# Kernel tuning notes

Hardware: AMD Instinct MI355X
Metric: run time of the kernel (lower is better)

Reference implementation:

```python
import jax, jax.numpy as jnp
import numpy as np

B, DIM, HEADS, AGENT = 32, 768, 12, 49
H0 = W0 = 28
N = H0 * W0


def setup_inputs() -> dict:
    key = jax.random.key(0)
    ks = jax.random.split(key, 24)
    p = lambda i, shape: jax.random.normal(ks[i], shape, jnp.float32) * 0.02
    return {
        "rgb_fea": jax.random.normal(ks[0], (B, N, DIM), jnp.float32),
        "depth_fea": jax.random.normal(ks[1], (B, N, DIM), jnp.float32),
        "rgb_q_w": p(2, (DIM, DIM)), "rgb_kv_w": p(3, (DIM, 2 * DIM)),
        "rgb_proj_w": p(4, (DIM, DIM)), "rgb_proj_b": jnp.zeros((DIM,), jnp.float32),
        "depth_q_w": p(5, (DIM, DIM)), "depth_kv_w": p(6, (DIM, 2 * DIM)),
        "depth_proj_w": p(7, (DIM, DIM)), "depth_proj_b": jnp.zeros((DIM,), jnp.float32),
        "rgb_dwc_w": p(8, (3, 3, 1, DIM)), "rgb_dwc_b": jnp.zeros((DIM,), jnp.float32),
        "depth_dwc_w": p(9, (3, 3, 1, DIM)), "depth_dwc_b": jnp.zeros((DIM,), jnp.float32),
        "rgb_an_bias": p(10, (HEADS, AGENT, 7, 7)), "rgb_na_bias": p(11, (HEADS, AGENT, 7, 7)),
        "rgb_ah_bias": p(12, (1, HEADS, AGENT, H0, 1)), "rgb_aw_bias": p(13, (1, HEADS, AGENT, 1, W0)),
        "rgb_ha_bias": p(14, (1, HEADS, H0, 1, AGENT)), "rgb_wa_bias": p(15, (1, HEADS, 1, W0, AGENT)),
        "depth_an_bias": p(16, (HEADS, AGENT, 7, 7)), "depth_na_bias": p(17, (HEADS, AGENT, 7, 7)),
        "depth_ah_bias": p(18, (1, HEADS, AGENT, H0, 1)), "depth_aw_bias": p(19, (1, HEADS, AGENT, 1, W0)),
        "depth_ha_bias": p(20, (1, HEADS, H0, 1, AGENT)), "depth_wa_bias": p(21, (1, HEADS, 1, W0, AGENT)),
        "H": H0, "W": W0,
    }


def _dwc(x, w, bias):
    # depthwise 3x3 conv, padding=1. x: [b,H,W,c], w: [3,3,1,c]
    y = jax.lax.conv_general_dilated(
        x, w, (1, 1), "SAME",
        dimension_numbers=("NHWC", "HWIO", "NHWC"),
        feature_group_count=x.shape[-1])
    return y + bias


def reference(rgb_fea, depth_fea, rgb_q_w, rgb_kv_w, rgb_proj_w, rgb_proj_b,
              depth_q_w, depth_kv_w, depth_proj_w, depth_proj_b,
              rgb_dwc_w, rgb_dwc_b, depth_dwc_w, depth_dwc_b,
              rgb_an_bias, rgb_na_bias, rgb_ah_bias, rgb_aw_bias, rgb_ha_bias, rgb_wa_bias,
              depth_an_bias, depth_na_bias, depth_ah_bias, depth_aw_bias, depth_ha_bias, depth_wa_bias,
              H, W):
    b, n, c = rgb_fea.shape
    heads = HEADS
    hd = c // heads
    scale = hd ** -0.5
    agent = AGENT
    ps = int(agent ** 0.5)  # 7x7 agent grid via adaptive avg pool (exact since H % ps == 0)

    rgb_q = rgb_fea @ rgb_q_w
    depth_q = depth_fea @ depth_q_w
    rgb_kv = (rgb_fea @ rgb_kv_w).reshape(b, n, 2, c)
    depth_kv = (depth_fea @ depth_kv_w).reshape(b, n, 2, c)

    heads_split = lambda t: t.reshape(b, -1, heads, hd).transpose(0, 2, 1, 3)  # [b,h,n,d]
    pool = lambda q: q.reshape(b, ps, H // ps, ps, W // ps, c).mean(axis=(2, 4)).reshape(b, agent, c)

    rgb_qh = heads_split(rgb_q)
    rgb_kh = heads_split(rgb_kv[:, :, 0])
    rgb_vh = heads_split(rgb_kv[:, :, 1])
    depth_qh = heads_split(depth_q)
    depth_kh = heads_split(depth_kv[:, :, 0])
    depth_vh = heads_split(depth_kv[:, :, 1])
    rgb_ah = heads_split(pool(rgb_q))      # [b,h,agent,d]
    depth_ah = heads_split(pool(depth_q))

    def pos_bias(an, ah_b, aw_b):
        # agent->native bias: interpolate 7x7 -> HxW (bilinear, half-pixel = torch align_corners=False)
        p1 = jax.image.resize(an, (heads, agent, H, W), method="linear").reshape(1, heads, agent, H * W)
        p2 = (ah_b + aw_b).reshape(1, heads, agent, H * W)
        return p1 + p2

    def ag_bias(na, ha_b, wa_b):
        # native->agent bias
        b1 = jax.image.resize(na, (heads, agent, H, W), method="linear").reshape(1, heads, agent, H * W).transpose(0, 1, 3, 2)
        b2 = (ha_b + wa_b).reshape(1, heads, H * W, agent)
        return b1 + b2

    rgb_pb = pos_bias(rgb_an_bias, rgb_ah_bias, rgb_aw_bias)
    depth_pb = pos_bias(depth_an_bias, depth_ah_bias, depth_aw_bias)

    # agent aggregation (cross-modal): depth agents attend to rgb k/v and vice versa
    depth_agent_attn = jax.nn.softmax(jnp.einsum("bhad,bhnd->bhan", depth_ah * scale, rgb_kh) + rgb_pb, axis=-1)
    depth_agent_v = jnp.einsum("bhan,bhnd->bhad", depth_agent_attn, rgb_vh)
    rgb_agent_attn = jax.nn.softmax(jnp.einsum("bhad,bhnd->bhan", rgb_ah * scale, depth_kh) + depth_pb, axis=-1)
    rgb_agent_v = jnp.einsum("bhan,bhnd->bhad", rgb_agent_attn, depth_vh)

    rgb_ab = ag_bias(rgb_na_bias, rgb_ha_bias, rgb_wa_bias)
    depth_ab = ag_bias(depth_na_bias, depth_ha_bias, depth_wa_bias)

    # agent broadcast: native queries attend to the other modality's agents
    rgb_q_attn = jax.nn.softmax(jnp.einsum("bhnd,bhad->bhna", rgb_qh * scale, depth_ah) + depth_ab, axis=-1)
    rgb_out = jnp.einsum("bhna,bhad->bhnd", rgb_q_attn, depth_agent_v)
    depth_q_attn = jax.nn.softmax(jnp.einsum("bhnd,bhad->bhna", depth_qh * scale, rgb_ah) + rgb_ab, axis=-1)
    depth_out = jnp.einsum("bhna,bhad->bhnd", depth_q_attn, rgb_agent_v)

    merge = lambda t: t.transpose(0, 2, 1, 3).reshape(b, n, c)
    rgb_out = merge(rgb_out) + _dwc(merge(rgb_vh).reshape(b, H, W, c), rgb_dwc_w, rgb_dwc_b).reshape(b, n, c)
    depth_out = merge(depth_out) + _dwc(merge(depth_vh).reshape(b, H, W, c), depth_dwc_w, depth_dwc_b).reshape(b, n, c)

    rgb_out = rgb_out @ rgb_proj_w + rgb_proj_b
    depth_out = depth_out @ depth_proj_w + depth_proj_b
    return rgb_out, depth_out
```

## Files before the change

kernel.cpp:

```cpp
#include <hip/hip_runtime.h>
#include <hip/hip_bf16.h>

#define BATCH 32
#define NPOS 784
#define DIM 768
#define HEADS 12
#define HD 64
#define AGENT 49
#define HH 28
#define WW 28
#define MROWS (BATCH*NPOS)
#define SCALE 0.125f

using bf16 = __hip_bfloat16;
typedef __attribute__((ext_vector_type(4))) float f32x4;
typedef __attribute__((ext_vector_type(8))) short short8v;

__device__ __forceinline__ float bf2f(bf16 x) { return __bfloat162float(x); }
__device__ __forceinline__ float bfs2f(short s) {
    unsigned int u = ((unsigned int)(unsigned short)s) << 16;
    return __uint_as_float(u);
}
__device__ __forceinline__ unsigned short f2bf(float x) {
    unsigned int u = __float_as_uint(x);
    unsigned int r = (u + 0x7fffu + ((u >> 16) & 1u)) >> 16;
    return (unsigned short)r;
}

#define GLOAD_LDS16(g, l) __builtin_amdgcn_global_load_lds( \
    (const __attribute__((address_space(1))) unsigned int*)(g), \
    (__attribute__((address_space(3))) unsigned int*)(l), 16, 0, 0)

__global__ __launch_bounds__(256) void convert_bf16(
    const float* __restrict__ src, bf16* __restrict__ dst, int n8)
{
    int idx = blockIdx.x * 256 + threadIdx.x;
    if (idx >= n8) return;
    const float* p = src + (size_t)idx * 8;
    float4 r0 = *reinterpret_cast<const float4*>(p);
    float4 r1 = *reinterpret_cast<const float4*>(p + 4);
    short8v v;
    v[0] = (short)f2bf(r0.x); v[1] = (short)f2bf(r0.y);
    v[2] = (short)f2bf(r0.z); v[3] = (short)f2bf(r0.w);
    v[4] = (short)f2bf(r1.x); v[5] = (short)f2bf(r1.y);
    v[6] = (short)f2bf(r1.z); v[7] = (short)f2bf(r1.w);
    *reinterpret_cast<short8v*>((short*)dst + (size_t)idx * 8) = v;
}

__global__ __launch_bounds__(256) void transpose_w_bf16(
    const float* __restrict__ W, bf16* __restrict__ Wt, int K, int N)
{
    __shared__ float t[32][33];
    int tx = threadIdx.x & 31, ty = threadIdx.x >> 5;
    int k0 = blockIdx.y * 32, n0 = blockIdx.x * 32;
#pragma unroll
    for (int i = 0; i < 4; ++i)
        t[ty + 8 * i][tx] = W[(size_t)(k0 + ty + 8 * i) * N + n0 + tx];
    __syncthreads();
#pragma unroll
    for (int i = 0; i < 4; ++i)
        Wt[(size_t)(n0 + ty + 8 * i) * K + k0 + tx] = __float2bfloat16(t[tx][ty + 8 * i]);
}

template<bool OUTF32>
__global__ __launch_bounds__(256) void gemm_mfma(
    const bf16* __restrict__ A, const bf16* __restrict__ Bt,
    const float* __restrict__ bias, void* __restrict__ Cp,
    int M, int N, int K)
{
    __shared__ __align__(16) short As[128 * 64];
    __shared__ __align__(16) short Bs[128 * 64];

    int tid = threadIdx.x;
    int wave = tid >> 6, lane = tid & 63;

    int gx = gridDim.x;
    int nwg = gx * gridDim.y;
    int bid = blockIdx.y * gx + blockIdx.x;
    int cpx = nwg >> 3;
    int nb = (bid & 7) * cpx + (bid >> 3);
    int m0 = (nb / gx) * 128, n0 = (nb % gx) * 128;

    int wm = (wave >> 1) * 64, wn = (wave & 1) * 64;
    int acol = lane & 15, kgrp = lane >> 4;

    f32x4 acc[4][4] = {};
    const short* Ab = (const short*)A;
    const short* Btb = (const short*)Bt;

    for (int k0 = 0; k0 < K; k0 += 64) {
#pragma unroll
        for (int it = 0; it < 4; ++it) {
            int idx = tid + 256 * it;
            int row = idx >> 3, seg = idx & 7;
            int sseg = seg ^ (row & 7);
            GLOAD_LDS16(Ab + (size_t)(m0 + row) * K + k0 + sseg * 8, &As[idx * 8]);
        }
#pragma unroll
        for (int it = 0; it < 4; ++it) {
            int idx = tid + 256 * it;
            int row = idx >> 3, seg = idx & 7;
            int sseg = seg ^ (row & 7);
            GLOAD_LDS16(Btb + (size_t)(n0 + row) * K + k0 + sseg * 8, &Bs[idx * 8]);
        }
        __syncthreads();

#pragma unroll
        for (int kk = 0; kk < 2; ++kk) {
            short8v af[4], bfr[4];
#pragma unroll
            for (int mf = 0; mf < 4; ++mf) {
                int row = wm + mf * 16 + acol;
                int seg = (kk * 4 + kgrp) ^ (row & 7);
                af[mf] = *reinterpret_cast<const short8v*>(&As[row * 64 + seg * 8]);
            }
#pragma unroll
            for (int nf = 0; nf < 4; ++nf) {
                int row = wn + nf * 16 + acol;
                int seg = (kk * 4 + kgrp) ^ (row & 7);
                bfr[nf] = *reinterpret_cast<const short8v*>(&Bs[row * 64 + seg * 8]);
            }
#pragma unroll
            for (int mf = 0; mf < 4; ++mf)
#pragma unroll
                for (int nf = 0; nf < 4; ++nf)
                    acc[mf][nf] = __builtin_amdgcn_mfma_f32_16x16x32_bf16(
                        af[mf], bfr[nf], acc[mf][nf], 0, 0, 0);
        }
        __syncthreads();
    }

    int rgrp = kgrp * 4, cidx = acol;
#pragma unroll
    for (int mf = 0; mf < 4; ++mf)
#pragma unroll
        for (int nf = 0; nf < 4; ++nf)
#pragma unroll
            for (int r = 0; r < 4; ++r) {
                int row = m0 + wm + mf * 16 + rgrp + r;
                int col = n0 + wn + nf * 16 + cidx;
                float v = acc[mf][nf][r];
                if constexpr (OUTF32)
                    ((float*)Cp)[(size_t)row * N + col] = v + bias[col];
                else
                    ((bf16*)Cp)[(size_t)row * N + col] = __float2bfloat16(v);
            }
}

__global__ void pool_kernel(const bf16* __restrict__ q, float* __restrict__ ahp)
{
    int idx = blockIdx.x * 256 + threadIdx.x;
    if (idx >= BATCH * AGENT * DIM) return;
    int c = idx % DIM;
    int a = (idx / DIM) % AGENT;
    int b = idx / (DIM * AGENT);
    int ai = a / 7, aj = a % 7;
    float s = 0.f;
#pragma unroll
    for (int u = 0; u < 4; ++u)
#pragma unroll
        for (int v = 0; v < 4; ++v) {
            int n = (ai * 4 + u) * WW + (aj * 4 + v);
            s += bf2f(q[((size_t)b * NPOS + n) * DIM + c]);
        }
    ahp[idx] = s * (1.f / 16.f);
}

__device__ __forceinline__ float bilerp7(const float* __restrict__ img, int i, int j)
{
    float si = 0.25f * i - 0.375f, sj = 0.25f * j - 0.375f;
    int i0 = (int)floorf(si); float fi = si - i0;
    int j0 = (int)floorf(sj); float fj = sj - j0;
    int i0c = min(max(i0, 0), 6), i1c = min(max(i0 + 1, 0), 6);
    int j0c = min(max(j0, 0), 6), j1c = min(max(j0 + 1, 0), 6);
    float v00 = img[i0c * 7 + j0c], v01 = img[i0c * 7 + j1c];
    float v10 = img[i1c * 7 + j0c], v11 = img[i1c * 7 + j1c];
    return (1.f - fi) * ((1.f - fj) * v00 + fj * v01) + fi * ((1.f - fj) * v10 + fj * v11);
}

__global__ void pos_bias_kernel(const float* __restrict__ an, const float* __restrict__ ah_b,
                                const float* __restrict__ aw_b, bf16* __restrict__ pb)
{
    int idx = blockIdx.x * 256 + threadIdx.x;
    if (idx >= HEADS * AGENT * NPOS) return;
    int n = idx % NPOS;
    int a = (idx / NPOS) % AGENT;
    int h = idx / (NPOS * AGENT);
    int i = n / WW, j = n % WW;
    float v = bilerp7(an + (size_t)(h * AGENT + a) * 49, i, j);
    v += ah_b[(h * AGENT + a) * HH + i] + aw_b[(h * AGENT + a) * WW + j];
    pb[idx] = __float2bfloat16(v);
}

__global__ void ag_bias_kernel(const float* __restrict__ na, const float* __restrict__ ha_b,
                               const float* __restrict__ wa_b, bf16* __restrict__ ab)
{
    int idx = blockIdx.x * 256 + threadIdx.x;
    if (idx >= HEADS * NPOS * AGENT) return;
    int a = idx % AGENT;
    int n = (idx / AGENT) % NPOS;
    int h = idx / (AGENT * NPOS);
    int i = n / WW, j = n % WW;
    float v = bilerp7(na + (size_t)(h * AGENT + a) * 49, i, j);
    v += ha_b[(h * HH + i) * AGENT + a] + wa_b[(h * WW + j) * AGENT + a];
    ab[idx] = __float2bfloat16(v);
}

__global__ __launch_bounds__(256, 2) void agent_attn3(
    const float* __restrict__ ahp, const bf16* __restrict__ kv,
    const bf16* __restrict__ pb, bf16* __restrict__ agent_v)
{
    __shared__ __align__(16) char smem[75776];
    short (*pL)[64][72]  = (short (*)[64][72])smem;
    short (*VtL)[64][72] = (short (*)[64][72])(smem + 36864);
    float (*Om)[64][66]  = (float (*)[64][66])smem;
    float (*mw)[64]      = (float (*)[64])(smem + 73728);
    float (*lw)[64]      = (float (*)[64])(smem + 74752);

    int tid = threadIdx.x;
    int wave = tid >> 6, lane = tid & 63;
    int acol = lane & 15, kgrp = lane >> 4;
    int h = blockIdx.x % HEADS;
    int b = blockIdx.x / HEADS;
    const short* kvs = (const short*)kv;
    const bf16* pbh = pb + (size_t)h * AGENT * NPOS;

    short8v qa[2][4];
#pragma unroll
    for (int ks = 0; ks < 2; ++ks)
#pragma unroll
        for (int mf = 0; mf < 4; ++mf) {
            int a = mf * 16 + acol;
            short8v v = {};
            if (a < AGENT) {
                const float* src = ahp + ((size_t)b * AGENT + a) * DIM + h * HD + ks * 32 + kgrp * 8;
                float4 r0 = *reinterpret_cast<const float4*>(src);
                float4 r1 = *reinterpret_cast<const float4*>(src + 4);
                v[0] = (short)f2bf(r0.x * SCALE); v[1] = (short)f2bf(r0.y * SCALE);
                v[2] = (short)f2bf(r0.z * SCALE); v[3] = (short)f2bf(r0.w * SCALE);
                v[4] = (short)f2bf(r1.x * SCALE); v[5] = (short)f2bf(r1.y * SCALE);
                v[6] = (short)f2bf(r1.z * SCALE); v[7] = (short)f2bf(r1.w * SCALE);
            }
            qa[ks][mf] = v;
        }

    float mrun[16], lrun[16];
#pragma unroll
    for (int i = 0; i < 16; ++i) { mrun[i] = -1e30f; lrun[i] = 0.f; }
    f32x4 accO[4][4] = {};

    for (int t = wave; t < 13; t += 4) {
        int n0 = t * 64;
        {
            int p = lane & 31, dh = lane >> 5;
            const short* v0p = kvs + (size_t)(b * NPOS + n0 + 2 * p) * (2 * DIM) + DIM + h * HD + dh * 32;
#pragma unroll
            for (int s = 0; s < 4; ++s) {
                short8v va = {}, vb = {};
                if (n0 + 2 * p < NPOS)     va = *reinterpret_cast<const short8v*>(v0p + s * 8);
                if (n0 + 2 * p + 1 < NPOS) vb = *reinterpret_cast<const short8v*>(v0p + 2 * DIM + s * 8);
#pragma unroll
                for (int u = 0; u < 8; ++u) {
                    int d = dh * 32 + s * 8 + u;
                    unsigned int w = ((unsigned int)(unsigned short)va[u]) |
                                     (((unsigned int)(unsigned short)vb[u]) << 16);
                    *reinterpret_cast<unsigned int*>(&VtL[wave][d][2 * p]) = w;
                }
            }
        }

        short8v kb[2][4];
#pragma unroll
        for (int nf = 0; nf < 4; ++nf) {
            int n = n0 + nf * 16 + acol;
            bool val = (n < NPOS);
            const short* kp = kvs + (size_t)(b * NPOS + n) * (2 * DIM) + h * HD + kgrp * 8;
#pragma unroll
            for (int ks = 0; ks < 2; ++ks) {
                short8v v = {};
                if (val) v = *reinterpret_cast<const short8v*>(kp + ks * 32);
                kb[ks][nf] = v;
            }
        }

        f32x4 accS[4][4] = {};
#pragma unroll
        for (int mf = 0; mf < 4; ++mf)
#pragma unroll
            for (int nf = 0; nf < 4; ++nf) {
                accS[mf][nf] = __builtin_amdgcn_mfma_f32_16x16x32_bf16(qa[0][mf], kb[0][nf], accS[mf][nf], 0, 0, 0);
                accS[mf][nf] = __builtin_amdgcn_mfma_f32_16x16x32_bf16(qa[1][mf], kb[1][nf], accS[mf][nf], 0, 0, 0);
            }

#pragma unroll
        for (int mf = 0; mf < 4; ++mf)
#pragma unroll
            for (int r = 0; r < 4; ++r) {
                int a = mf * 16 + kgrp * 4 + r;
                float s[4];
                float mt = -1e30f;
#pragma unroll
                for (int nf = 0; nf < 4; ++nf) {
                    int n = n0 + nf * 16 + acol;
                    float sv = -1e30f;
                    if (n < NPOS) {
                        sv = accS[mf][nf][r];
                        if (a < AGENT) sv += bf2f(pbh[(size_t)a * NPOS + n]);
                    }
                    s[nf] = sv;
                    mt = fmaxf(mt, sv);
                }
#pragma unroll
                for (int off = 1; off < 16; off <<= 1)
                    mt = fmaxf(mt, __shfl_xor(mt, off));
                float mnew = fmaxf(mrun[mf * 4 + r], mt);
                float fac = __expf(mrun[mf * 4 + r] - mnew);
                float ps = 0.f;
#pragma unroll
                for (int nf = 0; nf < 4; ++nf) {
                    float pv = (s[nf] > -1e29f) ? __expf(s[nf] - mnew) : 0.f;
                    ps += pv;
                    pL[wave][a][nf * 16 + acol] = (short)f2bf(pv);
                }
#pragma unroll
                for (int off = 1; off < 16; off <<= 1)
                    ps += __shfl_xor(ps, off);
                mrun[mf * 4 + r] = mnew;
                lrun[mf * 4 + r] = lrun[mf * 4 + r] * fac + ps;
#pragma unroll
                for (int df = 0; df < 4; ++df) accO[mf][df][r] *= fac;
            }

        short8v vb2[2][4];
#pragma unroll
        for (int ks = 0; ks < 2; ++ks)
#pragma unroll
            for (int df = 0; df < 4; ++df)
                vb2[ks][df] = *reinterpret_cast<const short8v*>(
                    &VtL[wave][df * 16 + acol][ks * 32 + kgrp * 8]);
#pragma unroll
        for (int mf = 0; mf < 4; ++mf) {
#pragma unroll
            for (int ks = 0; ks < 2; ++ks) {
                short8v pa = *reinterpret_cast<const short8v*>(
                    &pL[wave][mf * 16 + acol][ks * 32 + kgrp * 8]);
#pragma unroll
                for (int df = 0; df < 4; ++df)
                    accO[mf][df] = __builtin_amdgcn_mfma_f32_16x16x32_bf16(pa, vb2[ks][df], accO[mf][df], 0, 0, 0);
            }
        }
    }

    if (acol == 0) {
#pragma unroll
        for (int mf = 0; mf < 4; ++mf)
#pragma unroll
            for (int r = 0; r < 4; ++r) {
                mw[wave][mf * 16 + kgrp * 4 + r] = mrun[mf * 4 + r];
                lw[wave][mf * 16 + kgrp * 4 + r] = lrun[mf * 4 + r];
            }
    }
    __syncthreads();
#pragma unroll
    for (int mf = 0; mf < 4; ++mf)
#pragma unroll
        for (int df = 0; df < 4; ++df)
#pragma unroll
            for (int r = 0; r < 4; ++r)
                Om[wave][mf * 16 + kgrp * 4 + r][df * 16 + acol] = accO[mf][df][r];
    __syncthreads();

    for (int idx = tid; idx < AGENT * HD; idx += 256) {
        int a = idx >> 6, d = idx & 63;
        float m = fmaxf(fmaxf(mw[0][a], mw[1][a]), fmaxf(mw[2][a], mw[3][a]));
        float l = 0.f, o = 0.f;
#pragma unroll
        for (int w = 0; w < 4; ++w) {
            float f = __expf(mw[w][a] - m);
            l += f * lw[w][a];
            o += f * Om[w][a][d];
        }
        ((short*)agent_v)[(((size_t)b * HEADS + h) * AGENT + a) * HD + d] = (short)f2bf(o / l);
    }
}

__global__ __launch_bounds__(256) void q_attn_mfma(
    bf16* qpre, const bf16* __restrict__ kv_own,
    const float* __restrict__ ahp_x, const bf16* __restrict__ ab_x,
    const bf16* __restrict__ agv_x,
    const float* __restrict__ dwc_w, const float* __restrict__ dwc_b)
{
    __shared__ short pL[4][16][72];
    __shared__ float oL[4][16][68];
    __shared__ float wS[9][64];
    __shared__ float cbS[64];

    int blk = blockIdx.x;
    int half = blk & 1;
    int h = (blk >> 1) % HEADS;
    int b = blk / (2 * HEADS);
    int tid = threadIdx.x;
    int wave = tid >> 6, lane = tid & 63;
    int acol = lane & 15, kgrp = lane >> 4;

    for (int i = tid; i < 9 * 64; i += 256)
        wS[i >> 6][i & 63] = dwc_w[(i >> 6) * DIM + h * HD + (i & 63)];
    if (tid < 64) cbS[tid] = dwc_b[h * HD + tid];
    for (int i = tid; i < 4 * 16 * 72; i += 256)
        ((short*)pL)[i] = 0;

    short8v bs[2][4];
#pragma unroll
    for (int ks = 0; ks < 2; ++ks)
#pragma unroll
        for (int nf = 0; nf < 4; ++nf) {
            int a = nf * 16 + acol;
            short8v v = {};
            if (a < AGENT) {
                const float* src = ahp_x + ((size_t)b * AGENT + a) * DIM + h * HD + ks * 32 + kgrp * 8;
                float4 r0 = *reinterpret_cast<const float4*>(src);
                float4 r1 = *reinterpret_cast<const float4*>(src + 4);
                v[0] = (short)f2bf(r0.x * SCALE); v[1] = (short)f2bf(r0.y * SCALE);
                v[2] = (short)f2bf(r0.z * SCALE); v[3] = (short)f2bf(r0.w * SCALE);
                v[4] = (short)f2bf(r1.x * SCALE); v[5] = (short)f2bf(r1.y * SCALE);
                v[6] = (short)f2bf(r1.z * SCALE); v[7] = (short)f2bf(r1.w * SCALE);
            }
            bs[ks][nf] = v;
        }

    const short* agvs = (const short*)agv_x;
    short8v bv[2][4];
#pragma unroll
    for (int ks = 0; ks < 2; ++ks)
#pragma unroll
        for (int nf = 0; nf < 4; ++nf) {
            int d = nf * 16 + acol;
            short8v v = {};
#pragma unroll
            for (int i = 0; i < 8; ++i) {
                int a = ks * 32 + kgrp * 8 + i;
                if (a < AGENT)
                    v[i] = agvs[(((size_t)b * HEADS + h) * AGENT + a) * HD + d];
            }
            bv[ks][nf] = v;
        }

    __syncthreads();

    int tstart = half ? 25 : 0, tend = half ? 49 : 25;
    for (int t = tstart + wave; t < tend; t += 4) {
        int n0 = t * 16;
        const short* qrow = (const short*)qpre +
            ((size_t)(b * NPOS + n0 + acol)) * DIM + h * HD + kgrp * 8;
        short8v a0 = *reinterpret_cast<const short8v*>(qrow);
        short8v a1 = *reinterpret_cast<const short8v*>(qrow + 32);

        f32x4 accs[4] = {};
#pragma unroll
        for (int nf = 0; nf < 4; ++nf) {
            accs[nf] = __builtin_amdgcn_mfma_f32_16x16x32_bf16(a0, bs[0][nf], accs[nf], 0, 0, 0);
            accs[nf] = __builtin_amdgcn_mfma_f32_16x16x32_bf16(a1, bs[1][nf], accs[nf], 0, 0, 0);
        }

        float inv[4];
#pragma unroll
        for (int r = 0; r < 4; ++r) {
            int n = n0 + kgrp * 4 + r;
            float sarr[4];
            float m = -1e30f;
#pragma unroll
            for (int nf = 0; nf < 4; ++nf) {
                int a = nf * 16 + acol;
                float s = -1e30f;
                if (a < AGENT)
                    s = accs[nf][r] + bf2f(ab_x[((size_t)h * NPOS + n) * AGENT + a]);
                sarr[nf] = s;
                m = fmaxf(m, s);
            }
#pragma unroll
            for (int off = 1; off < 16; off <<= 1)
                m = fmaxf(m, __shfl_xor(m, off));
            float ls = 0.f;
#pragma unroll
            for (int nf = 0; nf < 4; ++nf) {
                float p = (sarr[nf] > -1e29f) ? __expf(sarr[nf] - m) : 0.f;
                sarr[nf] = p;
                ls += p;
            }
#pragma unroll
            for (int off = 1; off < 16; off <<= 1)
                ls += __shfl_xor(ls, off);
            inv[r] = 1.f / ls;
#pragma unroll
            for (int nf = 0; nf < 4; ++nf) {
                int a = nf * 16 + acol;
                if (a < AGENT)
                    pL[wave][kgrp * 4 + r][a] = (short)f2bf(sarr[nf]);
            }
        }

        short8v p0 = *reinterpret_cast<const short8v*>(&pL[wave][acol][kgrp * 8]);
        short8v p1 = *reinterpret_cast<const short8v*>(&pL[wave][acol][kgrp * 8 + 32]);

        f32x4 acco[4] = {};
#pragma unroll
        for (int nf = 0; nf < 4; ++nf) {
            acco[nf] = __builtin_amdgcn_mfma_f32_16x16x32_bf16(p0, bv[0][nf], acco[nf], 0, 0, 0);
            acco[nf] = __builtin_amdgcn_mfma_f32_16x16x32_bf16(p1, bv[1][nf], acco[nf], 0, 0, 0);
        }

#pragma unroll
        for (int r = 0; r < 4; ++r)
#pragma unroll
            for (int nf = 0; nf < 4; ++nf)
                oL[wave][kgrp * 4 + r][nf * 16 + acol] = acco[nf][r] * inv[r];

#pragma unroll
        for (int it2 = 0; it2 < 2; ++it2) {
            int item = lane + 64 * it2;
            int rl = item >> 3, d8 = item & 7;
            int n = n0 + rl;
            int i = n / WW, j = n % WW;
            float accv[8];
            {
                float4 o0 = *reinterpret_cast<const float4*>(&oL[wave][rl][d8 * 8]);
                float4 o1 = *reinterpret_cast<const float4*>(&oL[wave][rl][d8 * 8 + 4]);
                accv[0] = o0.x + cbS[d8 * 8 + 0]; accv[1] = o0.y + cbS[d8 * 8 + 1];
                accv[2] = o0.z + cbS[d8 * 8 + 2]; accv[3] = o0.w + cbS[d8 * 8 + 3];
                accv[4] = o1.x + cbS[d8 * 8 + 4]; accv[5] = o1.y + cbS[d8 * 8 + 5];
                accv[6] = o1.z + cbS[d8 * 8 + 6]; accv[7] = o1.w + cbS[d8 * 8 + 7];
            }
#pragma unroll
            for (int di = -1; di <= 1; ++di) {
                int ii = i + di;
                if (ii < 0 || ii >= HH) continue;
#pragma unroll
                for (int dj = -1; dj <= 1; ++dj) {
                    int jj = j + dj;
                    if (jj < 0 || jj >= WW) continue;
                    short8v vv = *reinterpret_cast<const short8v*>(
                        (const short*)kv_own + ((size_t)(b * NPOS + ii * WW + jj)) * (2 * DIM) + DIM + h * HD + d8 * 8);
                    int tap = (di + 1) * 3 + (dj + 1);
#pragma unroll
                    for (int u = 0; u < 8; ++u)
                        accv[u] += wS[tap][d8 * 8 + u] * bfs2f(vv[u]);
                }
            }
            short8v ov;
#pragma unroll
            for (int u = 0; u < 8; ++u) ov[u] = (short)f2bf(accv[u]);
            *reinterpret_cast<short8v*>((short*)qpre +
                ((size_t)(b * NPOS + n)) * DIM + h * HD + d8 * 8) = ov;
        }
    }
}

extern "C" void kernel_launch(void* const* d_in, const int* in_sizes, int n_in,
                              void* d_out, int out_size, void* d_ws, size_t ws_size,
                              hipStream_t stream)
{
    const float* rgb_fea    = (const float*)d_in[0];
    const float* depth_fea  = (const float*)d_in[1];
    const float* rgb_q_w    = (const float*)d_in[2];
    const float* rgb_kv_w   = (const float*)d_in[3];
    const float* rgb_proj_w = (const float*)d_in[4];
    const float* rgb_proj_b = (const float*)d_in[5];
    const float* depth_q_w    = (const float*)d_in[6];
    const float* depth_kv_w   = (const float*)d_in[7];
    const float* depth_proj_w = (const float*)d_in[8];
    const float* depth_proj_b = (const float*)d_in[9];
    const float* rgb_dwc_w   = (const float*)d_in[10];
    const float* rgb_dwc_b   = (const float*)d_in[11];
    const float* depth_dwc_w = (const float*)d_in[12];
    const float* depth_dwc_b = (const float*)d_in[13];
    const float* rgb_an   = (const float*)d_in[14];
    const float* rgb_na   = (const float*)d_in[15];
    const float* rgb_ah_b = (const float*)d_in[16];
    const float* rgb_aw_b = (const float*)d_in[17];
    const float* rgb_ha_b = (const float*)d_in[18];
    const float* rgb_wa_b = (const float*)d_in[19];
    const float* depth_an   = (const float*)d_in[20];
    const float* depth_na   = (const float*)d_in[21];
    const float* depth_ah_b = (const float*)d_in[22];
    const float* depth_aw_b = (const float*)d_in[23];
    const float* depth_ha_b = (const float*)d_in[24];
    const float* depth_wa_b = (const float*)d_in[25];

    char* ws = (char*)d_ws;
    size_t off = 0;
    auto alloc = [&](size_t bytes) -> void* {
        void* p = ws + off;
        off += (bytes + 255) & ~(size_t)255;
        return p;
    };
    bf16* rgb_q    = (bf16*)alloc((size_t)MROWS * DIM * 2);
    bf16* depth_q  = (bf16*)alloc((size_t)MROWS * DIM * 2);
    bf16* rgb_kv   = (bf16*)alloc((size_t)MROWS * 2 * DIM * 2);
    bf16* depth_kv = (bf16*)alloc((size_t)MROWS * 2 * DIM * 2);
    bf16* rgb_pb    = (bf16*)alloc((size_t)HEADS * AGENT * NPOS * 2);
    bf16* depth_pb  = (bf16*)alloc((size_t)HEADS * AGENT * NPOS * 2);
    bf16* rgb_ab    = (bf16*)alloc((size_t)HEADS * NPOS * AGENT * 2);
    bf16* depth_ab  = (bf16*)alloc((size_t)HEADS * NPOS * AGENT * 2);
    bf16* rgb_agv   = (bf16*)alloc((size_t)BATCH * HEADS * AGENT * HD * 2);
    bf16* depth_agv = (bf16*)alloc((size_t)BATCH * HEADS * AGENT * HD * 2);
    bf16* proj_wt_r = (bf16*)alloc((size_t)DIM * DIM * 2);
    bf16* proj_wt_d = (bf16*)alloc((size_t)DIM * DIM * 2);
    size_t ubase = off;
    bf16* q_wt_r  = (bf16*)alloc((size_t)DIM * DIM * 2);
    bf16* kv_wt_r = (bf16*)alloc((size_t)DIM * 2 * DIM * 2);
    bf16* q_wt_d  = (bf16*)alloc((size_t)DIM * DIM * 2);
    bf16* kv_wt_d = (bf16*)alloc((size_t)DIM * 2 * DIM * 2);
    off = ubase;
    float* rgb_ahp   = (float*)alloc((size_t)BATCH * AGENT * DIM * 4);
    float* depth_ahp = (float*)alloc((size_t)BATCH * AGENT * DIM * 4);

    bf16* fea_bf_r = (bf16*)d_out;
    bf16* fea_bf_d = fea_bf_r + (size_t)MROWS * DIM;

    dim3 blk(256);
    int n8 = MROWS * DIM / 8;

    convert_bf16<<<(n8 + 255) / 256, blk, 0, stream>>>(rgb_fea, fea_bf_r, n8);
    convert_bf16<<<(n8 + 255) / 256, blk, 0, stream>>>(depth_fea, fea_bf_d, n8);
    transpose_w_bf16<<<dim3(24, 24), blk, 0, stream>>>(rgb_q_w, q_wt_r, DIM, DIM);
    transpose_w_bf16<<<dim3(48, 24), blk, 0, stream>>>(rgb_kv_w, kv_wt_r, DIM, 2 * DIM);
    transpose_w_bf16<<<dim3(24, 24), blk, 0, stream>>>(depth_q_w, q_wt_d, DIM, DIM);
    transpose_w_bf16<<<dim3(48, 24), blk, 0, stream>>>(depth_kv_w, kv_wt_d, DIM, 2 * DIM);
    transpose_w_bf16<<<dim3(24, 24), blk, 0, stream>>>(rgb_proj_w, proj_wt_r, DIM, DIM);
    transpose_w_bf16<<<dim3(24, 24), blk, 0, stream>>>(depth_proj_w, proj_wt_d, DIM, DIM);

    gemm_mfma<false><<<dim3(6, 196), blk, 0, stream>>>(fea_bf_r, q_wt_r, nullptr, rgb_q, MROWS, DIM, DIM);
    gemm_mfma<false><<<dim3(6, 196), blk, 0, stream>>>(fea_bf_d, q_wt_d, nullptr, depth_q, MROWS, DIM, DIM);
    gemm_mfma<false><<<dim3(12, 196), blk, 0, stream>>>(fea_bf_r, kv_wt_r, nullptr, rgb_kv, MROWS, 2 * DIM, DIM);
    gemm_mfma<false><<<dim3(12, 196), blk, 0, stream>>>(fea_bf_d, kv_wt_d, nullptr, depth_kv, MROWS, 2 * DIM, DIM);

    pool_kernel<<<(BATCH * AGENT * DIM + 255) / 256, blk, 0, stream>>>(rgb_q, rgb_ahp);
    pool_kernel<<<(BATCH * AGENT * DIM + 255) / 256, blk, 0, stream>>>(depth_q, depth_ahp);

    pos_bias_kernel<<<(HEADS * AGENT * NPOS + 255) / 256, blk, 0, stream>>>(rgb_an, rgb_ah_b, rgb_aw_b, rgb_pb);
    pos_bias_kernel<<<(HEADS * AGENT * NPOS + 255) / 256, blk, 0, stream>>>(depth_an, depth_ah_b, depth_aw_b, depth_pb);
    ag_bias_kernel<<<(HEADS * NPOS * AGENT + 255) / 256, blk, 0, stream>>>(rgb_na, rgb_ha_b, rgb_wa_b, rgb_ab);
    ag_bias_kernel<<<(HEADS * NPOS * AGENT + 255) / 256, blk, 0, stream>>>(depth_na, depth_ha_b, depth_wa_b, depth_ab);

    agent_attn3<<<BATCH * HEADS, blk, 0, stream>>>(depth_ahp, rgb_kv, rgb_pb, depth_agv);
    agent_attn3<<<BATCH * HEADS, blk, 0, stream>>>(rgb_ahp, depth_kv, depth_pb, rgb_agv);

    q_attn_mfma<<<BATCH * HEADS * 2, blk, 0, stream>>>(rgb_q, rgb_kv, depth_ahp, depth_ab, depth_agv,
                                                       rgb_dwc_w, rgb_dwc_b);
    q_attn_mfma<<<BATCH * HEADS * 2, blk, 0, stream>>>(depth_q, depth_kv, rgb_ahp, rgb_ab, rgb_agv,
                                                       depth_dwc_w, depth_dwc_b);

    float* out = (float*)d_out;
    gemm_mfma<true><<<dim3(6, 196), blk, 0, stream>>>(rgb_q, proj_wt_r, rgb_proj_b, out, MROWS, DIM, DIM);
    gemm_mfma<true><<<dim3(6, 196), blk, 0, stream>>>(depth_q, proj_wt_d, depth_proj_b,
                                                      out + (size_t)MROWS * DIM, MROWS, DIM, DIM);
}
```

Before: 729.7 us.

## Double-buffer LDS tiles in MFMA GEMM to overlap global loads with compute

The GEMM kernel now keeps two LDS buffers for the A and B tiles. It issues the direct-to-LDS global loads for the next K tile before running the MFMA work on the current one, then waits on vmcnt and a barrier before swapping buffers. This hides global load latency behind matrix math, where before each step loaded, synced and only then computed. In exchange LDS use doubles to 64KB per block, which may reduce how many blocks fit per CU.

```diff
diff --git a/kernel.cpp b/kernel.cpp
--- a/kernel.cpp
+++ b/kernel.cpp
@@ -68,8 +68,8 @@
     const float* __restrict__ bias, void* __restrict__ Cp,
     int M, int N, int K)
 {
-    __shared__ __align__(16) short As[128 * 64];
-    __shared__ __align__(16) short Bs[128 * 64];
+    __shared__ __align__(16) short As[2][128 * 64];
+    __shared__ __align__(16) short Bs[2][128 * 64];
 
     int tid = threadIdx.x;
     int wave = tid >> 6, lane = tid & 63;
@@ -88,22 +88,34 @@
     const short* Ab = (const short*)A;
     const short* Btb = (const short*)Bt;
 
-    for (int k0 = 0; k0 < K; k0 += 64) {
+    auto STAGE = [&](int buf, int k0) {
 #pragma unroll
         for (int it = 0; it < 4; ++it) {
             int idx = tid + 256 * it;
             int row = idx >> 3, seg = idx & 7;
             int sseg = seg ^ (row & 7);
-            GLOAD_LDS16(Ab + (size_t)(m0 + row) * K + k0 + sseg * 8, &As[idx * 8]);
+            GLOAD_LDS16(Ab + (size_t)(m0 + row) * K + k0 + sseg * 8, &As[buf][idx * 8]);
         }
 #pragma unroll
         for (int it = 0; it < 4; ++it) {
             int idx = tid + 256 * it;
             int row = idx >> 3, seg = idx & 7;
             int sseg = seg ^ (row & 7);
-            GLOAD_LDS16(Btb + (size_t)(n0 + row) * K + k0 + sseg * 8, &Bs[idx * 8]);
-        }
-        __syncthreads();
+            GLOAD_LDS16(Btb + (size_t)(n0 + row) * K + k0 + sseg * 8, &Bs[buf][idx * 8]);
+        }
+    };
+
+    int nt = K >> 6;
+    int cur = 0;
+
+    STAGE(0, 0);
+    asm volatile("s_waitcnt vmcnt(0)" ::: "memory");
+    __builtin_amdgcn_sched_barrier(0);
+    __builtin_amdgcn_s_barrier();
+    __builtin_amdgcn_sched_barrier(0);
+
+    for (int t = 0; t < nt; ++t) {
+        if (t + 1 < nt) STAGE(cur ^ 1, (t + 1) << 6);
 
 #pragma unroll
         for (int kk = 0; kk < 2; ++kk) {
@@ -112,13 +124,13 @@
             for (int mf = 0; mf < 4; ++mf) {
                 int row = wm + mf * 16 + acol;
                 int seg = (kk * 4 + kgrp) ^ (row & 7);
-                af[mf] = *reinterpret_cast<const short8v*>(&As[row * 64 + seg * 8]);
+                af[mf] = *reinterpret_cast<const short8v*>(&As[cur][row * 64 + seg * 8]);
             }
 #pragma unroll
             for (int nf = 0; nf < 4; ++nf) {
                 int row = wn + nf * 16 + acol;
                 int seg = (kk * 4 + kgrp) ^ (row & 7);
-                bfr[nf] = *reinterpret_cast<const short8v*>(&Bs[row * 64 + seg * 8]);
+                bfr[nf] = *reinterpret_cast<const short8v*>(&Bs[cur][row * 64 + seg * 8]);
             }
 #pragma unroll
             for (int mf = 0; mf < 4; ++mf)
@@ -127,7 +139,14 @@
                     acc[mf][nf] = __builtin_amdgcn_mfma_f32_16x16x32_bf16(
                         af[mf], bfr[nf], acc[mf][nf], 0, 0, 0);
         }
-        __syncthreads();
+
+        if (t + 1 < nt) {
+            asm volatile("s_waitcnt vmcnt(0)" ::: "memory");
+            __builtin_amdgcn_sched_barrier(0);
+            __builtin_amdgcn_s_barrier();
+            __builtin_amdgcn_sched_barrier(0);
+            cur ^= 1;
+        }
     }
 
     int rgrp = kgrp * 4, cidx = acol;
```

After: 754.7 us. 1.03x slower.
